# Kernel tuning notes

Measured on AMD Instinct MI355X. Metric: run time of the kernel, lower is better.

## Reference

```python
import jax, jax.numpy as jnp
import numpy as np

ALPHA = 3.0   # self.alpha
TAU = 0.1     # contrastive temperature
K = 8         # configs.k (top-k hyperedges per node)


def _scale(x, w, ehy, enod):
    """One scale of incidence_matrix_learn.
    x: [B, L, D] series tokens; w: [ws, D] word tokens;
    ehy: [H, D] hyperedge embedding table; enod: [N, D] node embedding table, N = L + ws.
    Returns (binary incidence matrix [N, H] float32, scalar contrastive loss).
    """
    B = x.shape[0]
    # concat_all[i]: cat(x.permute(0,2,1), word_expanded) -> [B, D, N]
    we = jnp.broadcast_to(w.T[None], (B,) + w.T.shape)          # [B, D, ws]
    concat = jnp.concatenate([jnp.transpose(x, (0, 2, 1)), we], axis=-1)  # [B, D, N]
    N, H = enod.shape[0], ehy.shape[0]
    # adjacency: softmax(relu(alpha * nodeec @ hyperen.T)) along hyperedge dim
    a = enod @ ehy.T                                            # [N, H]
    adj = jax.nn.softmax(jax.nn.relu(ALPHA * a), axis=-1)
    # top-k mask + threshold > 0.5 -> binary incidence matrix
    k = min(H, K)
    _, idx = jax.lax.top_k(adj, k)                              # [N, k]
    mask = jnp.zeros_like(adj).at[jnp.arange(N)[:, None], idx].set(1.0)
    adj_bin = ((adj * mask) > 0.5).astype(jnp.float32)          # [N, H]
    # positives: nodes sharing any hyperedge (build_pos_indices_from_edge_index),
    # equivalent to (A A^T > 0) with self excluded; dropping all-zero columns is a no-op here
    P = (adj_bin @ adj_bin.T > 0) & ~jnp.eye(N, dtype=bool)     # [N, N]
    cnt = P.sum(axis=1)                                         # positives per node
    # acl_loss_batched, vectorized over batch and nodes
    nodes = jnp.transpose(concat, (0, 2, 1))                    # [B, N, D]
    nrm = nodes / jnp.maximum(jnp.linalg.norm(nodes, axis=-1, keepdims=True), 1e-12)
    sim = jnp.einsum('bnd,bmd->bnm', nrm, nrm) / TAU            # [B, N, N]
    denom = jax.nn.logsumexp(sim, axis=-1)                      # [B, N]
    pos_mean = jnp.einsum('bnm,nm->bn', sim, P.astype(sim.dtype)) / jnp.maximum(cnt, 1)
    valid = cnt > 0                                             # [N]
    loss_sum = jnp.sum(jnp.where(valid[None, :], denom - pos_mean, 0.0))
    vc = B * valid.sum()
    loss = jnp.where(vc > 0, loss_sum / jnp.maximum(vc, 1), 0.0)
    return adj_bin, loss


def setup_inputs() -> dict:
    key = jax.random.key(0)
    ks = jax.random.split(key, 8)
    B, D = 64, 512
    return dict(
        x0=jax.random.normal(ks[0], (B, 512, D), dtype=jnp.float32),
        x1=jax.random.normal(ks[1], (B, 256, D), dtype=jnp.float32),
        word0=jax.random.normal(ks[2], (128, D), dtype=jnp.float32),
        word1=jax.random.normal(ks[3], (128, D), dtype=jnp.float32),
        embhy0=jax.random.normal(ks[4], (128, D), dtype=jnp.float32),
        embhy1=jax.random.normal(ks[5], (64, D), dtype=jnp.float32),
        embnod0=jax.random.normal(ks[6], (640, D), dtype=jnp.float32),
        embnod1=jax.random.normal(ks[7], (384, D), dtype=jnp.float32),
    )


def reference(x0, x1, word0, word1, embhy0, embhy1, embnod0, embnod1):
    a0, l0 = _scale(x0, word0, embhy0, embnod0)
    a1, l1 = _scale(x1, word1, embhy1, embnod1)
    return (a0, a1, l0 + l1)
```

## Files before the change

### kernel.cpp

```cpp
#include <hip/hip_runtime.h>


#define DDIM 512
#define BATCH 64

typedef __attribute__((ext_vector_type(8))) short short8;
typedef __attribute__((ext_vector_type(4))) float f32x4;

__device__ __forceinline__ unsigned short f2bf(float f) {
  unsigned int u = __float_as_uint(f);
  u += 0x7fffu + ((u >> 16) & 1u);
  return (unsigned short)(u >> 16);
}

__device__ __forceinline__ void async16(const void* g, void* l) {
  __builtin_amdgcn_global_load_lds(
      (const __attribute__((address_space(1))) unsigned int*)g,
      (__attribute__((address_space(3))) unsigned int*)l, 16, 0, 0);
}

__global__ __launch_bounds__(256) void prep_kernel(
    const float* __restrict__ enod0, const float* __restrict__ ehy0,
    const float* __restrict__ enod1, const float* __restrict__ ehy1,
    float* __restrict__ adj0, float* __restrict__ adj1,
    int* __restrict__ labels0, int* __restrict__ labels1,
    const float* __restrict__ x0, const float* __restrict__ w0,
    const float* __restrict__ x1, const float* __restrict__ w1,
    unsigned short* __restrict__ nhat0, unsigned short* __restrict__ nhat1,
    float* __restrict__ acc) {
  const int t = threadIdx.x;
  if (blockIdx.x < 1024) {
    if (blockIdx.x == 0 && t == 0) { acc[0] = 0.f; acc[1] = 0.f; }
    const bool s0 = blockIdx.x < 640;
    const int n = s0 ? blockIdx.x : blockIdx.x - 640;
    const int H = s0 ? 128 : 64;
    const float* enod = s0 ? enod0 : enod1;
    const float* ehy = s0 ? ehy0 : ehy1;
    float* out_adj = s0 ? adj0 : adj1;
    int* labels = s0 ? labels0 : labels1;
    __shared__ float erow[DDIM];
    __shared__ float red[128];
    __shared__ int lab;
    if (t < 128) ((float4*)erow)[t] = ((const float4*)(enod + (size_t)n * DDIM))[t];
    if (t == 0) lab = -1;
    __syncthreads();
    float v = 0.f;
    if (t < H) {
      const float4* hr = (const float4*)(ehy + (size_t)t * DDIM);
      float a = 0.f;
      #pragma unroll 8
      for (int d = 0; d < DDIM / 4; ++d) {
        float4 h = hr[d];
        float4 e = ((const float4*)erow)[d];
        a = fmaf(h.x, e.x, a); a = fmaf(h.y, e.y, a);
        a = fmaf(h.z, e.z, a); a = fmaf(h.w, e.w, a);
      }
      v = fmaxf(0.f, 3.0f * a);
    }
    if (t < 128) red[t] = v;
    __syncthreads();
    for (int s = 64; s > 0; s >>= 1) {
      if (t < s) red[t] = fmaxf(red[t], red[t + s]);
      __syncthreads();
    }
    const float mx = red[0];
    __syncthreads();
    const float e = (t < H) ? __expf(v - mx) : 0.f;
    if (t < 128) red[t] = e;
    __syncthreads();
    for (int s = 64; s > 0; s >>= 1) {
      if (t < s) red[t] += red[t + s];
      __syncthreads();
    }
    const float sum = red[0];
    if (t < H) {
      const float adj = e / sum;
      const float bin = (adj > 0.5f) ? 1.0f : 0.0f;
      out_adj[(size_t)n * H + t] = bin;
      if (bin > 0.f) lab = t;
    }
    __syncthreads();
    if (t == 0) labels[n] = lab;
  } else {
    const int wave = t >> 6;
    const int lane = t & 63;
    const int g = (blockIdx.x - 1024) * 4 + wave;
    const bool s0 = g < BATCH * 640;
    const int gg = s0 ? g : g - BATCH * 640;
    const int N = s0 ? 640 : 384;
    const int L = s0 ? 512 : 256;
    const float* x = s0 ? x0 : x1;
    const float* w = s0 ? w0 : w1;
    unsigned short* nhat = s0 ? nhat0 : nhat1;
    const int b = gg / N;
    const int n = gg - b * N;
    const float* src = (n < L) ? (x + ((size_t)b * L + n) * DDIM)
                               : (w + (size_t)(n - L) * DDIM);
    const float4* rowp = (const float4*)src;
    const float4 v0 = rowp[lane];
    const float4 v1 = rowp[lane + 64];
    float ss = v0.x * v0.x + v0.y * v0.y + v0.z * v0.z + v0.w * v0.w +
               v1.x * v1.x + v1.y * v1.y + v1.z * v1.z + v1.w * v1.w;
    #pragma unroll
    for (int off = 32; off > 0; off >>= 1) ss += __shfl_xor(ss, off);
    const float rinv = 1.0f / fmaxf(sqrtf(ss), 1e-12f);
    ushort4 o0, o1;
    o0.x = f2bf(v0.x * rinv); o0.y = f2bf(v0.y * rinv);
    o0.z = f2bf(v0.z * rinv); o0.w = f2bf(v0.w * rinv);
    o1.x = f2bf(v1.x * rinv); o1.y = f2bf(v1.y * rinv);
    o1.z = f2bf(v1.z * rinv); o1.w = f2bf(v1.w * rinv);
    ushort4* op = (ushort4*)(nhat + ((size_t)b * N + n) * DDIM);
    op[lane] = o0;
    op[lane + 64] = o1;
  }
}

__global__ __launch_bounds__(256) void cnt_kernel(
    const int* __restrict__ labels0, int* __restrict__ cnt0,
    const int* __restrict__ labels1, int* __restrict__ cnt1,
    int* __restrict__ valid) {
  const bool s0 = blockIdx.x == 0;
  const int* labels = s0 ? labels0 : labels1;
  int* cnt = s0 ? cnt0 : cnt1;
  int* validcnt = s0 ? valid : valid + 1;
  const int N = s0 ? 640 : 384;
  __shared__ int lab[640];
  __shared__ int hist[128];
  __shared__ int vc;
  const int t = threadIdx.x;
  if (t == 0) vc = 0;
  if (t < 128) hist[t] = 0;
  for (int i = t; i < N; i += 256) lab[i] = labels[i];
  __syncthreads();
  for (int i = t; i < N; i += 256)
    if (lab[i] >= 0) atomicAdd(&hist[lab[i]], 1);
  __syncthreads();
  int lv = 0;
  for (int i = t; i < N; i += 256) {
    const int c = (lab[i] >= 0) ? hist[lab[i]] - 1 : 0;
    cnt[i] = c;
    if (c > 0) ++lv;
  }
  if (lv > 0) atomicAdd(&vc, lv);
  __syncthreads();
  if (t == 0) *validcnt = vc;
}

__global__ __launch_bounds__(128, 2) void lse_kernel(
    const unsigned short* __restrict__ nhat0, const int* __restrict__ labels0,
    const int* __restrict__ cnt0, const unsigned short* __restrict__ nhat1,
    const int* __restrict__ labels1, const int* __restrict__ cnt1,
    float* __restrict__ loss_acc) {
  __shared__ short8 Bbuf[2][1024];
  __shared__ int labS[640];
  __shared__ float redS[64];
  __shared__ float redP[64];
  const int tid = threadIdx.x;
  const bool s0 = blockIdx.x < 640;
  const int i = s0 ? blockIdx.x : blockIdx.x - 640;
  const int N = s0 ? 640 : 384;
  const int ntiles = s0 ? 10 : 6;
  const unsigned short* nhat = s0 ? nhat0 : nhat1;
  const int* labels = s0 ? labels0 : labels1;
  const int* cnt = s0 ? cnt0 : cnt1;
  float* acc_out = s0 ? loss_acc : loss_acc + 1;
  const int b = i & 63;
  const int tn = i >> 6;
  const int n0 = tn * 64;
  const int wave = tid >> 6;
  const int lane = tid & 63;
  const int lrow = lane & 15;
  const int lq = lane >> 4;
  for (int t = tid; t < N; t += 128) labS[t] = labels[t];

  const size_t base = (size_t)b * N * DDIM;
  const int rw0 = n0 + wave * 32;
  const unsigned short* Ap0 = nhat + base + (size_t)(rw0 + lrow) * DDIM + lq * 8;
  const unsigned short* Ap1 = nhat + base + (size_t)(rw0 + 16 + lrow) * DDIM + lq * 8;
  short8 a0[16], a1[16];
  #pragma unroll
  for (int ks = 0; ks < 16; ++ks) {
    a0[ks] = *(const short8*)(Ap0 + ks * 32);
    a1[ks] = *(const short8*)(Ap1 + ks * 32);
  }

  const int f0 = wave * 8;
  #pragma unroll
  for (int fi = 0; fi < 8; ++fi) {
    const int f = f0 + fi;
    const int j = f >> 2, ks = f & 3;
    const unsigned short* g = nhat + base +
        (size_t)(j * 16 + lrow) * DDIM + ks * 32 + lq * 8;
    async16(g, &Bbuf[0][f * 64]);
  }
  __syncthreads();

  int labn[2][4];
  #pragma unroll
  for (int s = 0; s < 2; ++s)
    #pragma unroll
    for (int r = 0; r < 4; ++r) labn[s][r] = labS[rw0 + s * 16 + lq * 4 + r];

  float se[2][4] = {{0.f, 0.f, 0.f, 0.f}, {0.f, 0.f, 0.f, 0.f}};
  float pos[2][4] = {{0.f, 0.f, 0.f, 0.f}, {0.f, 0.f, 0.f, 0.f}};
  const int nchunks = ntiles * 4;

  for (int mt = 0; mt < ntiles; ++mt) {
    f32x4 acc[4][2];
    #pragma unroll
    for (int j = 0; j < 4; ++j) {
      acc[j][0] = (f32x4){0.f, 0.f, 0.f, 0.f};
      acc[j][1] = (f32x4){0.f, 0.f, 0.f, 0.f};
    }
    #pragma unroll
    for (int kc = 0; kc < 4; ++kc) {
      const int nc = mt * 4 + kc + 1;
      if (nc < nchunks) {
        const int mt2 = nc >> 2, kc2 = nc & 3;
        short8* dst = &Bbuf[(kc + 1) & 1][0];
        #pragma unroll
        for (int fi = 0; fi < 8; ++fi) {
          const int f = f0 + fi;
          const int j = f >> 2, ks = f & 3;
          const unsigned short* g = nhat + base +
              (size_t)(mt2 * 64 + j * 16 + lrow) * DDIM +
              kc2 * 128 + ks * 32 + lq * 8;
          async16(g, dst + f * 64);
        }
      }
      const short8* bb = &Bbuf[kc & 1][0];
      #pragma unroll
      for (int ks = 0; ks < 4; ++ks) {
        const short8 b0 = bb[(0 + ks) * 64 + lane];
        const short8 b1 = bb[(4 + ks) * 64 + lane];
        const short8 b2 = bb[(8 + ks) * 64 + lane];
        const short8 b3 = bb[(12 + ks) * 64 + lane];
        const short8 av0 = a0[kc * 4 + ks];
        const short8 av1 = a1[kc * 4 + ks];
        acc[0][0] = __builtin_amdgcn_mfma_f32_16x16x32_bf16(av0, b0, acc[0][0], 0, 0, 0);
        acc[0][1] = __builtin_amdgcn_mfma_f32_16x16x32_bf16(av1, b0, acc[0][1], 0, 0, 0);
        acc[1][0] = __builtin_amdgcn_mfma_f32_16x16x32_bf16(av0, b1, acc[1][0], 0, 0, 0);
        acc[1][1] = __builtin_amdgcn_mfma_f32_16x16x32_bf16(av1, b1, acc[1][1], 0, 0, 0);
        acc[2][0] = __builtin_amdgcn_mfma_f32_16x16x32_bf16(av0, b2, acc[2][0], 0, 0, 0);
        acc[2][1] = __builtin_amdgcn_mfma_f32_16x16x32_bf16(av1, b2, acc[2][1], 0, 0, 0);
        acc[3][0] = __builtin_amdgcn_mfma_f32_16x16x32_bf16(av0, b3, acc[3][0], 0, 0, 0);
        acc[3][1] = __builtin_amdgcn_mfma_f32_16x16x32_bf16(av1, b3, acc[3][1], 0, 0, 0);
      }
      __syncthreads();
    }
    const int m0 = mt * 64;
    #pragma unroll
    for (int j = 0; j < 4; ++j) {
      const int m = m0 + j * 16 + lrow;
      const int labm = labS[m];
      #pragma unroll
      for (int s = 0; s < 2; ++s) {
        const int row0 = rw0 + s * 16 + lq * 4;
        #pragma unroll
        for (int r = 0; r < 4; ++r) {
          const float sim = acc[j][s][r] * 10.0f;
          se[s][r] += __expf(sim - 10.0f);
          if (labn[s][r] >= 0 && labm == labn[s][r] && m != row0 + r)
            pos[s][r] += sim;
        }
      }
    }
  }

  #pragma unroll
  for (int off = 1; off <= 8; off <<= 1) {
    #pragma unroll
    for (int s = 0; s < 2; ++s)
      #pragma unroll
      for (int r = 0; r < 4; ++r) {
        se[s][r] += __shfl_xor(se[s][r], off);
        pos[s][r] += __shfl_xor(pos[s][r], off);
      }
  }
  if (lrow == 0) {
    #pragma unroll
    for (int s = 0; s < 2; ++s)
      #pragma unroll
      for (int r = 0; r < 4; ++r) {
        redS[wave * 32 + s * 16 + lq * 4 + r] = se[s][r];
        redP[wave * 32 + s * 16 + lq * 4 + r] = pos[s][r];
      }
  }
  __syncthreads();
  if (tid < 64) {
    const int c = cnt[n0 + tid];
    if (c > 0)
      atomicAdd(acc_out, (10.0f + logf(redS[tid])) - redP[tid] / (float)c);
  }
}

__global__ void final_kernel(const float* __restrict__ acc,
                             const int* __restrict__ valid,
                             float* __restrict__ out) {
  float l = 0.f;
  if (valid[0] > 0) l += acc[0] / (float)(BATCH * valid[0]);
  if (valid[1] > 0) l += acc[1] / (float)(BATCH * valid[1]);
  out[0] = l;
}

extern "C" void kernel_launch(void* const* d_in, const int* in_sizes, int n_in,
                              void* d_out, int out_size, void* d_ws,
                              size_t ws_size, hipStream_t stream) {
  const float* x0 = (const float*)d_in[0];
  const float* x1 = (const float*)d_in[1];
  const float* w0 = (const float*)d_in[2];
  const float* w1 = (const float*)d_in[3];
  const float* ehy0 = (const float*)d_in[4];
  const float* ehy1 = (const float*)d_in[5];
  const float* enod0 = (const float*)d_in[6];
  const float* enod1 = (const float*)d_in[7];

  float* out = (float*)d_out;
  float* adj0 = out;
  float* adj1 = out + 640 * 128;
  float* lossp = out + 640 * 128 + 384 * 64;

  unsigned short* nhat0 = (unsigned short*)d_ws;
  unsigned short* nhat1 = nhat0 + (size_t)BATCH * 640 * DDIM;
  int* ip = (int*)(nhat1 + (size_t)BATCH * 384 * DDIM);
  int* labels0 = ip;
  int* labels1 = labels0 + 640;
  int* cnt0 = labels1 + 384;
  int* cnt1 = cnt0 + 640;
  int* valid = cnt1 + 384;
  float* acc = (float*)(valid + 2);

  prep_kernel<<<1024 + 16384, 256, 0, stream>>>(
      enod0, ehy0, enod1, ehy1, adj0, adj1, labels0, labels1,
      x0, w0, x1, w1, nhat0, nhat1, acc);
  cnt_kernel<<<2, 256, 0, stream>>>(labels0, cnt0, labels1, cnt1, valid);
  lse_kernel<<<1024, 128, 0, stream>>>(nhat0, labels0, cnt0, nhat1, labels1,
                                       cnt1, acc);
  final_kernel<<<1, 1, 0, stream>>>(acc, valid, lossp);
}
```

Before: 246.8 us.

## Exploit symmetry of similarity matrix to halve Gram-tile MFMA work

After: 249.5 us. Within noise of the previous version (+1.1%).

```diff
diff --git a/kernel.cpp b/kernel.cpp
--- a/kernel.cpp
+++ b/kernel.cpp
@@ -26,11 +26,9 @@
     int* __restrict__ labels0, int* __restrict__ labels1,
     const float* __restrict__ x0, const float* __restrict__ w0,
     const float* __restrict__ x1, const float* __restrict__ w1,
-    unsigned short* __restrict__ nhat0, unsigned short* __restrict__ nhat1,
-    float* __restrict__ acc) {
+    unsigned short* __restrict__ nhat0, unsigned short* __restrict__ nhat1) {
   const int t = threadIdx.x;
   if (blockIdx.x < 1024) {
-    if (blockIdx.x == 0 && t == 0) { acc[0] = 0.f; acc[1] = 0.f; }
     const bool s0 = blockIdx.x < 640;
     const int n = s0 ? blockIdx.x : blockIdx.x - 640;
     const int H = s0 ? 128 : 64;
@@ -146,27 +144,26 @@
   if (t == 0) *validcnt = vc;
 }
 
-__global__ __launch_bounds__(128, 2) void lse_kernel(
+__global__ __launch_bounds__(128, 1) void lse_kernel(
     const unsigned short* __restrict__ nhat0, const int* __restrict__ labels0,
-    const int* __restrict__ cnt0, const unsigned short* __restrict__ nhat1,
-    const int* __restrict__ labels1, const int* __restrict__ cnt1,
-    float* __restrict__ loss_acc) {
+    const unsigned short* __restrict__ nhat1, const int* __restrict__ labels1,
+    float* __restrict__ seG0, float* __restrict__ posG0,
+    float* __restrict__ seG1, float* __restrict__ posG1) {
   __shared__ short8 Bbuf[2][1024];
   __shared__ int labS[640];
-  __shared__ float redS[64];
-  __shared__ float redP[64];
   const int tid = threadIdx.x;
   const bool s0 = blockIdx.x < 640;
   const int i = s0 ? blockIdx.x : blockIdx.x - 640;
   const int N = s0 ? 640 : 384;
-  const int ntiles = s0 ? 10 : 6;
+  const int T = s0 ? 10 : 6;
   const unsigned short* nhat = s0 ? nhat0 : nhat1;
   const int* labels = s0 ? labels0 : labels1;
-  const int* cnt = s0 ? cnt0 : cnt1;
-  float* acc_out = s0 ? loss_acc : loss_acc + 1;
+  float* seG = s0 ? seG0 : seG1;
+  float* posG = s0 ? posG0 : posG1;
   const int b = i & 63;
   const int tn = i >> 6;
   const int n0 = tn * 64;
+  const int ntj = s0 ? ((tn < 5) ? 6 : 5) : ((tn < 3) ? 4 : 3);
   const int wave = tid >> 6;
   const int lane = tid & 63;
   const int lrow = lane & 15;
@@ -190,7 +187,7 @@
     const int f = f0 + fi;
     const int j = f >> 2, ks = f & 3;
     const unsigned short* g = nhat + base +
-        (size_t)(j * 16 + lrow) * DDIM + ks * 32 + lq * 8;
+        (size_t)(n0 + j * 16 + lrow) * DDIM + ks * 32 + lq * 8;
     async16(g, &Bbuf[0][f * 64]);
   }
   __syncthreads();
@@ -203,9 +200,11 @@
 
   float se[2][4] = {{0.f, 0.f, 0.f, 0.f}, {0.f, 0.f, 0.f, 0.f}};
   float pos[2][4] = {{0.f, 0.f, 0.f, 0.f}, {0.f, 0.f, 0.f, 0.f}};
-  const int nchunks = ntiles * 4;
-
-  for (int mt = 0; mt < ntiles; ++mt) {
+  const int nchunks = ntj * 4;
+
+  for (int jt = 0; jt < ntj; ++jt) {
+    int mt = tn + jt; if (mt >= T) mt -= T;
+    const int m0 = mt * 64;
     f32x4 acc[4][2];
     #pragma unroll
     for (int j = 0; j < 4; ++j) {
@@ -214,9 +213,10 @@
     }
     #pragma unroll
     for (int kc = 0; kc < 4; ++kc) {
-      const int nc = mt * 4 + kc + 1;
+      const int nc = jt * 4 + kc + 1;
       if (nc < nchunks) {
-        const int mt2 = nc >> 2, kc2 = nc & 3;
+        const int jt2 = nc >> 2, kc2 = nc & 3;
+        int mt2 = tn + jt2; if (mt2 >= T) mt2 -= T;
         short8* dst = &Bbuf[(kc + 1) & 1][0];
         #pragma unroll
         for (int fi = 0; fi < 8; ++fi) {
@@ -248,7 +248,8 @@
       }
       __syncthreads();
     }
-    const int m0 = mt * 64;
+    float colE[4] = {0.f, 0.f, 0.f, 0.f};
+    float colP[4] = {0.f, 0.f, 0.f, 0.f};
     #pragma unroll
     for (int j = 0; j < 4; ++j) {
       const int m = m0 + j * 16 + lrow;
@@ -259,9 +260,27 @@
         #pragma unroll
         for (int r = 0; r < 4; ++r) {
           const float sim = acc[j][s][r] * 10.0f;
-          se[s][r] += __expf(sim - 10.0f);
-          if (labn[s][r] >= 0 && labm == labn[s][r] && m != row0 + r)
-            pos[s][r] += sim;
+          const float e = __expf(sim - 10.0f);
+          const bool match =
+              labn[s][r] >= 0 && labm == labn[s][r] && m != row0 + r;
+          const float p = match ? sim : 0.f;
+          se[s][r] += e;
+          pos[s][r] += p;
+          colE[j] += e;
+          colP[j] += p;
+        }
+      }
+    }
+    if (jt > 0) {
+      #pragma unroll
+      for (int j = 0; j < 4; ++j) {
+        float ce = colE[j], cp = colP[j];
+        ce += __shfl_xor(ce, 16); ce += __shfl_xor(ce, 32);
+        cp += __shfl_xor(cp, 16); cp += __shfl_xor(cp, 32);
+        if (lq == 0) {
+          const int m = m0 + j * 16 + lrow;
+          atomicAdd(&seG[b * N + m], ce);
+          atomicAdd(&posG[b * N + m], cp);
         }
       }
     }
@@ -282,16 +301,36 @@
     for (int s = 0; s < 2; ++s)
       #pragma unroll
       for (int r = 0; r < 4; ++r) {
-        redS[wave * 32 + s * 16 + lq * 4 + r] = se[s][r];
-        redP[wave * 32 + s * 16 + lq * 4 + r] = pos[s][r];
-      }
-  }
-  __syncthreads();
-  if (tid < 64) {
-    const int c = cnt[n0 + tid];
-    if (c > 0)
-      atomicAdd(acc_out, (10.0f + logf(redS[tid])) - redP[tid] / (float)c);
-  }
+        const int row = rw0 + s * 16 + lq * 4 + r;
+        atomicAdd(&seG[b * N + row], se[s][r]);
+        atomicAdd(&posG[b * N + row], pos[s][r]);
+      }
+  }
+}
+
+__global__ __launch_bounds__(256) void reduce_kernel(
+    const float* __restrict__ seG0, const float* __restrict__ posG0,
+    const int* __restrict__ cnt0, const float* __restrict__ seG1,
+    const float* __restrict__ posG1, const int* __restrict__ cnt1,
+    float* __restrict__ acc) {
+  const int idx = blockIdx.x * 256 + threadIdx.x;
+  float v = 0.f;
+  int sel;
+  if (idx < BATCH * 640) {
+    sel = 0;
+    const int n = idx % 640;
+    const int c = cnt0[n];
+    if (c > 0) v = (10.0f + logf(seG0[idx])) - posG0[idx] / (float)c;
+  } else {
+    sel = 1;
+    const int k = idx - BATCH * 640;
+    const int n = k % 384;
+    const int c = cnt1[n];
+    if (c > 0) v = (10.0f + logf(seG1[k])) - posG1[k] / (float)c;
+  }
+  #pragma unroll
+  for (int off = 32; off > 0; off >>= 1) v += __shfl_xor(v, off);
+  if ((threadIdx.x & 63) == 0) atomicAdd(&acc[sel], v);
 }
 
 __global__ void final_kernel(const float* __restrict__ acc,
@@ -328,13 +367,22 @@
   int* cnt0 = labels1 + 384;
   int* cnt1 = cnt0 + 640;
   int* valid = cnt1 + 384;
-  float* acc = (float*)(valid + 2);
-
+  float* fz = (float*)(valid + 2);
+  float* seG0 = fz;
+  float* posG0 = seG0 + BATCH * 640;
+  float* seG1 = posG0 + BATCH * 640;
+  float* posG1 = seG1 + BATCH * 384;
+  float* acc = posG1 + BATCH * 384;
+
+  hipMemsetAsync(fz, 0,
+                 (size_t)(2 * BATCH * (640 + 384) + 2) * sizeof(float), stream);
   prep_kernel<<<1024 + 16384, 256, 0, stream>>>(
       enod0, ehy0, enod1, ehy1, adj0, adj1, labels0, labels1,
-      x0, w0, x1, w1, nhat0, nhat1, acc);
+      x0, w0, x1, w1, nhat0, nhat1);
   cnt_kernel<<<2, 256, 0, stream>>>(labels0, cnt0, labels1, cnt1, valid);
-  lse_kernel<<<1024, 128, 0, stream>>>(nhat0, labels0, cnt0, nhat1, labels1,
-                                       cnt1, acc);
+  lse_kernel<<<1024, 128, 0, stream>>>(nhat0, labels0, nhat1, labels1,
+                                       seG0, posG0, seG1, posG1);
+  reduce_kernel<<<256, 256, 0, stream>>>(seG0, posG0, cnt0, seG1, posG1, cnt1,
+                                         acc);
   final_kernel<<<1, 1, 0, stream>>>(acc, valid, lossp);
 }
```
